# Optimization experiments

Measured on AMD Instinct MI355X. Metric: run time of the kernel, lower is better.

The kernel has to match this reference:

```python
import jax, jax.numpy as jnp
import numpy as np

B, D, H, C = 128, 512, 1024, 1000


def setup_inputs() -> dict:
    key = jax.random.key(0)
    k1, k2, k3 = jax.random.split(key, 3)
    x = jax.random.normal(k1, (B, D), dtype=jnp.float32)
    W1 = jax.random.normal(k2, (D, H), dtype=jnp.float32) * (1.0 / np.sqrt(D))
    b1 = jnp.zeros((H,), dtype=jnp.float32)
    W2 = jax.random.normal(k3, (H, C), dtype=jnp.float32) * (1.0 / np.sqrt(H))
    b2 = jnp.zeros((C,), dtype=jnp.float32)
    return {"x": x, "W1": W1, "b1": b1, "W2": W2, "b2": b2, "step": 0}


def _logits(W1, b1, W2, b2, xi):
    # 2-layer MLP forward for a single sample xi: [D] -> [C]
    h = jnp.maximum(xi @ W1 + b1, 0.0)
    return h @ W2 + b2


def _per_sample_loss(params, xi, key):
    W1, b1, W2, b2 = params
    logit = _logits(W1, b1, W2, b2, xi)  # [C]
    # model samples a label from its own softmax (multinomial); sampling is
    # non-differentiable, matching torch's multinomial -> stop_gradient
    y = jax.random.categorical(key, jax.lax.stop_gradient(logit))
    return -jax.nn.log_softmax(logit)[y]  # CrossEntropyLoss on 1 sample


def reference(x, W1, b1, W2, b2, step):
    params = (W1, b1, W2, b2)
    keys = jax.random.split(jax.random.key(42), x.shape[0])
    # vmap(grad(loss)) -> per-sample gradients for every parameter
    grads = jax.vmap(jax.grad(_per_sample_loss), in_axes=(None, 0, 0))(params, x, keys)
    n = jnp.asarray(x.shape[0], dtype=x.dtype)
    # trace_p = sum_b ||g_b||^2 / B for each parameter
    traces = [jnp.sum(g * g) / n for g in grads]
    overall = traces[0] + traces[1] + traces[2] + traces[3]
    return jnp.stack([overall] + traces)  # [5]: overall, W1, b1, W2, b2
```

## Files before the change

kernel.cpp:

```cpp
#include <hip/hip_runtime.h>
#include <hip/hip_bf16.h>
#include <stdint.h>
#include <math.h>

#define B_N 128
#define D_N 512
#define H_N 1024
#define C_N 1000
#define CP  1024

__device__ __forceinline__ uint32_t rotl32(uint32_t v, int r) {
  return (v << r) | (v >> (32 - r));
}

__device__ __forceinline__ void threefry2x32(uint32_t k0, uint32_t k1,
                                             uint32_t x0, uint32_t x1,
                                             uint32_t &o0, uint32_t &o1) {
  uint32_t ks2 = k0 ^ k1 ^ 0x1BD11BDAu;
#define TF_R(r) { x0 += x1; x1 = rotl32(x1, r); x1 ^= x0; }
  x0 += k0; x1 += k1;
  TF_R(13) TF_R(15) TF_R(26) TF_R(6)
  x0 += k1; x1 += ks2 + 1u;
  TF_R(17) TF_R(29) TF_R(16) TF_R(24)
  x0 += ks2; x1 += k0 + 2u;
  TF_R(13) TF_R(15) TF_R(26) TF_R(6)
  x0 += k0; x1 += k1 + 3u;
  TF_R(17) TF_R(29) TF_R(16) TF_R(24)
  x0 += k1; x1 += ks2 + 4u;
  TF_R(13) TF_R(15) TF_R(26) TF_R(6)
  x0 += ks2; x1 += k0 + 5u;
#undef TF_R
  o0 = x0; o1 = x1;
}

__device__ __forceinline__ float gumbel_from_key(uint32_t k0, uint32_t k1, uint32_t i) {
  uint32_t o0, o1;
  threefry2x32(k0, k1, 0u, i, o0, o1);
  uint32_t bits = o0 ^ o1;
  uint32_t fb = (bits >> 9) | 0x3f800000u;
  float f = __uint_as_float(fb) - 1.0f;
  const float tiny = 1.1754943508222875e-38f;
  float u = fmaxf(tiny, f * (1.0f - tiny) + tiny);
  return -logf(-logf(u));
}

__device__ __forceinline__ float block_sum512(float v, float* red) {
  #pragma unroll
  for (int o = 32; o; o >>= 1) v += __shfl_xor(v, o);
  __syncthreads();
  if ((threadIdx.x & 63) == 0) red[threadIdx.x >> 6] = v;
  __syncthreads();
  return red[0] + red[1] + red[2] + red[3] + red[4] + red[5] + red[6] + red[7];
}

__device__ __forceinline__ float block_max512(float v, float* red) {
  #pragma unroll
  for (int o = 32; o; o >>= 1) v = fmaxf(v, __shfl_xor(v, o));
  __syncthreads();
  if ((threadIdx.x & 63) == 0) red[threadIdx.x >> 6] = v;
  __syncthreads();
  float m = red[0];
  #pragma unroll
  for (int w = 1; w < 8; w++) m = fmaxf(m, red[w]);
  return m;
}

__global__ __launch_bounds__(256) void k_fc1(const float* __restrict__ X,
                                             const float* __restrict__ W1,
                                             const float* __restrict__ b1,
                                             float* __restrict__ hpre) {
  __shared__ float xs[4 * D_N];
  int cbase = blockIdx.x * 128;
  int sbase = blockIdx.y * 4;
  int t = threadIdx.x;
  #pragma unroll
  for (int k = 0; k < 8; k++) {
    int idx = t + k * 256;
    int s = idx >> 9, d = idx & 511;
    xs[idx] = X[(sbase + s) * D_N + d];
  }
  __syncthreads();
  int c = cbase + (t & 127);
  int sq = t >> 7;
  const float* xp0 = &xs[(sq * 2 + 0) * D_N];
  const float* xp1 = &xs[(sq * 2 + 1) * D_N];
  float acc0 = 0.f, acc1 = 0.f;
  const float* W1c = W1 + c;
  for (int d0 = 0; d0 < D_N; d0 += 16) {
    float w[16];
    #pragma unroll
    for (int i = 0; i < 16; i++) w[i] = W1c[(d0 + i) * H_N];
    #pragma unroll
    for (int q = 0; q < 4; q++) {
      float4 xa = *reinterpret_cast<const float4*>(&xp0[d0 + q * 4]);
      float4 xb = *reinterpret_cast<const float4*>(&xp1[d0 + q * 4]);
      acc0 += xa.x * w[q*4+0] + xa.y * w[q*4+1] + xa.z * w[q*4+2] + xa.w * w[q*4+3];
      acc1 += xb.x * w[q*4+0] + xb.y * w[q*4+1] + xb.z * w[q*4+2] + xb.w * w[q*4+3];
    }
  }
  float bb = b1[c];
  int s0 = sbase + sq * 2;
  hpre[(s0 + 0) * H_N + c] = acc0 + bb;
  hpre[(s0 + 1) * H_N + c] = acc1 + bb;
}

__global__ __launch_bounds__(256) void k_fc2(const float* __restrict__ hpre,
                                             const float* __restrict__ W2,
                                             float* __restrict__ logits_part) {
  __shared__ float hs[8 * 512];
  int cbase = blockIdx.x * 128;
  int sbase = blockIdx.y * 8;
  int kb = blockIdx.z;
  int t = threadIdx.x;
  #pragma unroll
  for (int k = 0; k < 16; k++) {
    int idx = t + k * 256;
    int s = idx >> 9, j = idx & 511;
    hs[idx] = fmaxf(hpre[(sbase + s) * H_N + kb * 512 + j], 0.0f);
  }
  __syncthreads();
  int c = cbase + (t & 127);
  int sq = t >> 7;
  if (c < C_N) {
    const float* hp0 = &hs[(sq * 4 + 0) * 512];
    const float* hp1 = &hs[(sq * 4 + 1) * 512];
    const float* hp2 = &hs[(sq * 4 + 2) * 512];
    const float* hp3 = &hs[(sq * 4 + 3) * 512];
    float a0 = 0.f, a1 = 0.f, a2 = 0.f, a3 = 0.f;
    const float* W2c = W2 + (size_t)(kb * 512) * C_N + c;
    for (int j0 = 0; j0 < 512; j0 += 8) {
      float w[8];
      #pragma unroll
      for (int i = 0; i < 8; i++) w[i] = W2c[(j0 + i) * C_N];
      #pragma unroll
      for (int q = 0; q < 2; q++) {
        float4 hA = *reinterpret_cast<const float4*>(&hp0[j0 + q * 4]);
        float4 hB = *reinterpret_cast<const float4*>(&hp1[j0 + q * 4]);
        float4 hC = *reinterpret_cast<const float4*>(&hp2[j0 + q * 4]);
        float4 hD = *reinterpret_cast<const float4*>(&hp3[j0 + q * 4]);
        a0 += hA.x * w[q*4+0] + hA.y * w[q*4+1] + hA.z * w[q*4+2] + hA.w * w[q*4+3];
        a1 += hB.x * w[q*4+0] + hB.y * w[q*4+1] + hB.z * w[q*4+2] + hB.w * w[q*4+3];
        a2 += hC.x * w[q*4+0] + hC.y * w[q*4+1] + hC.z * w[q*4+2] + hC.w * w[q*4+3];
        a3 += hD.x * w[q*4+0] + hD.y * w[q*4+1] + hD.z * w[q*4+2] + hD.w * w[q*4+3];
      }
    }
    float* lp = logits_part + (size_t)kb * (B_N * CP);
    int s0 = sbase + sq * 4;
    lp[(s0 + 0) * CP + c] = a0;
    lp[(s0 + 1) * CP + c] = a1;
    lp[(s0 + 2) * CP + c] = a2;
    lp[(s0 + 3) * CP + c] = a3;
  }
}

__global__ __launch_bounds__(512) void k_sample(const float* __restrict__ X,
                                                const float* __restrict__ hpre,
                                                const float* __restrict__ logits_part,
                                                const float* __restrict__ b2,
                                                float* __restrict__ g,
                                                float* __restrict__ xsq_out,
                                                float* __restrict__ samp_part) {
  __shared__ float lg[C_N];
  __shared__ float red[8];
  __shared__ float redv[8];
  __shared__ int   redi[8];
  __shared__ uint32_t keys[2];
  int b = blockIdx.x;
  int t = threadIdx.x;

  const float* p0 = logits_part;
  const float* p1 = logits_part + (B_N * CP);
  lg[t] = p0[b * CP + t] + p1[b * CP + t] + b2[t];
  if (t + 512 < C_N)
    lg[t + 512] = p0[b * CP + t + 512] + p1[b * CP + t + 512] + b2[t + 512];
  if (t == 0) {
    uint32_t o0, o1;
    threefry2x32(0u, 42u, 0u, (uint32_t)b, o0, o1);
    keys[0] = o0; keys[1] = o1;
  }
  __syncthreads();
  uint32_t k0 = keys[0], k1 = keys[1];

  float bz = -INFINITY; int bi = 0x7fffffff;
  {
    float z0 = lg[t] + gumbel_from_key(k0, k1, (uint32_t)t);
    bz = z0; bi = t;
    if (t + 512 < C_N) {
      float z1 = lg[t + 512] + gumbel_from_key(k0, k1, (uint32_t)(t + 512));
      if (z1 > bz || (z1 == bz && (t + 512) < bi)) { bz = z1; bi = t + 512; }
    }
  }
  #pragma unroll
  for (int o = 32; o; o >>= 1) {
    float ov = __shfl_xor(bz, o);
    int   oi = __shfl_xor(bi, o);
    if (ov > bz || (ov == bz && oi < bi)) { bz = ov; bi = oi; }
  }
  if ((t & 63) == 0) { redv[t >> 6] = bz; redi[t >> 6] = bi; }
  __syncthreads();
  if (t == 0) {
    #pragma unroll
    for (int w = 1; w < 8; w++) {
      if (redv[w] > redv[0] || (redv[w] == redv[0] && redi[w] < redi[0])) {
        redv[0] = redv[w]; redi[0] = redi[w];
      }
    }
  }
  __syncthreads();
  int y = redi[0];

  float lm = lg[t];
  if (t + 512 < C_N) lm = fmaxf(lm, lg[t + 512]);
  float m = block_max512(lm, red);
  float ea = expf(lg[t] - m);
  float eb = (t + 512 < C_N) ? expf(lg[t + 512] - m) : 0.0f;
  float sum1 = block_sum512(ea + eb, red);
  float inv = 1.0f / sum1;

  float ga  = ea * inv - ((t == y) ? 1.0f : 0.0f);
  float gb2 = eb * inv - (((t + 512) == y) ? 1.0f : 0.0f);
  g[b * CP + t] = ga;
  g[b * CP + t + 512] = (t + 512 < C_N) ? gb2 : 0.0f;
  float gn = ga * ga + ((t + 512 < C_N) ? gb2 * gb2 : 0.0f);
  float tnorm = block_sum512(gn, red);

  float h0 = fmaxf(hpre[b * H_N + t], 0.0f);
  float h1 = fmaxf(hpre[b * H_N + t + 512], 0.0f);
  float hsq = block_sum512(h0 * h0 + h1 * h1, red);

  float xv = (t < D_N) ? X[b * D_N + t] : 0.0f;
  float xsq = block_sum512(xv * xv, red);

  if (t == 0) {
    xsq_out[b] = xsq;
    samp_part[b * 2 + 0] = hsq * tnorm;
    samp_part[b * 2 + 1] = tnorm;
  }
}

__global__ __launch_bounds__(512) void k_bwd1(const float* __restrict__ g,
                                              const float* __restrict__ W2,
                                              const float* __restrict__ hpre,
                                              const float* __restrict__ xsq,
                                              float* __restrict__ bwd_part) {
  __shared__ float gs[8 * 1024];
  __shared__ float xq[8];
  __shared__ float wred[8][2];
  int jb = blockIdx.x * 16;
  int sbase = blockIdx.y * 8;
  int t = threadIdx.x;
  #pragma unroll
  for (int k = 0; k < 16; k++) {
    int idx = t + k * 512;
    gs[idx] = g[(sbase + (idx >> 10)) * CP + (idx & 1023)];
  }
  if (t < 8) xq[t] = xsq[sbase + t];
  __syncthreads();

  int w = t >> 6, lane = t & 63;
  int j0 = jb + w * 2, j1 = j0 + 1;
  float a0[8] = {0,0,0,0,0,0,0,0};
  float a1[8] = {0,0,0,0,0,0,0,0};
  const float* w2r0 = W2 + (size_t)j0 * C_N;
  const float* w2r1 = W2 + (size_t)j1 * C_N;
  #pragma unroll
  for (int it = 0; it < 4; it++) {
    int c0 = it * 256 + lane * 4;
    bool act = (c0 < C_N);
    float4 wv0 = act ? *reinterpret_cast<const float4*>(w2r0 + c0)
                     : make_float4(0.f, 0.f, 0.f, 0.f);
    float4 wv1 = act ? *reinterpret_cast<const float4*>(w2r1 + c0)
                     : make_float4(0.f, 0.f, 0.f, 0.f);
    #pragma unroll
    for (int s = 0; s < 8; s++) {
      float4 gv = *reinterpret_cast<const float4*>(&gs[s * 1024 + c0]);
      a0[s] += wv0.x * gv.x + wv0.y * gv.y + wv0.z * gv.z + wv0.w * gv.w;
      a1[s] += wv1.x * gv.x + wv1.y * gv.y + wv1.z * gv.z + wv1.w * gv.w;
    }
  }
  #pragma unroll
  for (int off = 32; off; off >>= 1) {
    #pragma unroll
    for (int s = 0; s < 8; s++) {
      a0[s] += __shfl_xor(a0[s], off);
      a1[s] += __shfl_xor(a1[s], off);
    }
  }
  float cb = 0.f, cw = 0.f;
  #pragma unroll
  for (int s = 0; s < 8; s++) {
    float h0 = hpre[(sbase + s) * H_N + j0];
    float h1 = hpre[(sbase + s) * H_N + j1];
    float v0 = (h0 > 0.f) ? a0[s] : 0.f;
    float v1 = (h1 > 0.f) ? a1[s] : 0.f;
    float q = v0 * v0 + v1 * v1;
    cb += q;
    cw += xq[s] * q;
  }
  if (lane == 0) { wred[w][0] = cw; wred[w][1] = cb; }
  __syncthreads();
  if (t == 0) {
    float sw = 0.f, sb = 0.f;
    #pragma unroll
    for (int i = 0; i < 8; i++) { sw += wred[i][0]; sb += wred[i][1]; }
    int bid = blockIdx.y * 64 + blockIdx.x;
    bwd_part[bid * 2 + 0] = sw;
    bwd_part[bid * 2 + 1] = sb;
  }
}

__global__ __launch_bounds__(512) void k_final(const float* __restrict__ samp_part,
                                               const float* __restrict__ bwd_part,
                                               float* __restrict__ out) {
  __shared__ float red[8];
  int t = threadIdx.x;
  float w1v = bwd_part[t * 2 + 0] + bwd_part[(t + 512) * 2 + 0];
  float b1v = bwd_part[t * 2 + 1] + bwd_part[(t + 512) * 2 + 1];
  float w2v = (t < B_N) ? samp_part[t * 2 + 0] : 0.f;
  float b2v = (t < B_N) ? samp_part[t * 2 + 1] : 0.f;
  w1v = block_sum512(w1v, red);
  b1v = block_sum512(b1v, red);
  w2v = block_sum512(w2v, red);
  b2v = block_sum512(b2v, red);
  if (t == 0) {
    w1v /= 128.0f; b1v /= 128.0f; w2v /= 128.0f; b2v /= 128.0f;
    out[0] = w1v + b1v + w2v + b2v;
    out[1] = w1v;
    out[2] = b1v;
    out[3] = w2v;
    out[4] = b2v;
  }
}

extern "C" void kernel_launch(void* const* d_in, const int* in_sizes, int n_in,
                              void* d_out, int out_size, void* d_ws, size_t ws_size,
                              hipStream_t stream) {
  const float* X  = (const float*)d_in[0];
  const float* W1 = (const float*)d_in[1];
  const float* b1 = (const float*)d_in[2];
  const float* W2 = (const float*)d_in[3];
  const float* b2 = (const float*)d_in[4];
  float* out = (float*)d_out;

  float* ws        = (float*)d_ws;
  float* hpre      = ws;
  float* lpart     = hpre + 131072;
  float* g         = lpart + 262144;
  float* xsq       = g + 131072;
  float* samp_part = xsq + 128;
  float* bwd_part  = samp_part + 256;

  k_fc1<<<dim3(8, 32), 256, 0, stream>>>(X, W1, b1, hpre);
  k_fc2<<<dim3(8, 16, 2), 256, 0, stream>>>(hpre, W2, lpart);
  k_sample<<<B_N, 512, 0, stream>>>(X, hpre, lpart, b2, g, xsq, samp_part);
  k_bwd1<<<dim3(64, 16), 512, 0, stream>>>(g, W2, hpre, xsq, bwd_part);
  k_final<<<1, 512, 0, stream>>>(samp_part, bwd_part, out);
}
```

Measured before the change: 66.35 us.

## Split fc2 reduction into 8 K-partitions and double-buffer weight loads in fc1/fc2

fc2 now splits the hidden dimension into 8 partitions of 128 instead of 2 of 512, giving four times as many blocks. The sampling kernel sums 8 partial logit buffers. fc1 uses 512 threads with one sample per thread instead of two. Both GEMMs double-buffer weight registers to overlap global loads with FMAs. The trade is more partial-sum traffic and a larger workspace, in exchange for better parallelism and latency hiding.

Result: faster. 57.43 us (-13.4%).

```diff
diff --git a/kernel.cpp b/kernel.cpp
--- a/kernel.cpp
+++ b/kernel.cpp
@@ -8,6 +8,7 @@
 #define H_N 1024
 #define C_N 1000
 #define CP  1024
+#define NPART 8
 
 __device__ __forceinline__ uint32_t rotl32(uint32_t v, int r) {
   return (v << r) | (v >> (32 - r));
@@ -65,7 +66,7 @@
   return m;
 }
 
-__global__ __launch_bounds__(256) void k_fc1(const float* __restrict__ X,
+__global__ __launch_bounds__(512) void k_fc1(const float* __restrict__ X,
                                              const float* __restrict__ W1,
                                              const float* __restrict__ b1,
                                              float* __restrict__ hpre) {
@@ -74,83 +75,97 @@
   int sbase = blockIdx.y * 4;
   int t = threadIdx.x;
   #pragma unroll
-  for (int k = 0; k < 8; k++) {
-    int idx = t + k * 256;
-    int s = idx >> 9, d = idx & 511;
-    xs[idx] = X[(sbase + s) * D_N + d];
+  for (int k = 0; k < 4; k++) {
+    int idx = t + k * 512;
+    xs[idx] = X[(sbase + (idx >> 9)) * D_N + (idx & 511)];
   }
   __syncthreads();
   int c = cbase + (t & 127);
-  int sq = t >> 7;
-  const float* xp0 = &xs[(sq * 2 + 0) * D_N];
-  const float* xp1 = &xs[(sq * 2 + 1) * D_N];
-  float acc0 = 0.f, acc1 = 0.f;
+  const float* xp = &xs[(t >> 7) * D_N];
   const float* W1c = W1 + c;
-  for (int d0 = 0; d0 < D_N; d0 += 16) {
-    float w[16];
-    #pragma unroll
-    for (int i = 0; i < 16; i++) w[i] = W1c[(d0 + i) * H_N];
+  float wA[16], wB[16];
+  #pragma unroll
+  for (int i = 0; i < 16; i++) wA[i] = W1c[i * H_N];
+  float acc = 0.f;
+  for (int d0 = 0; d0 < D_N; d0 += 32) {
+    #pragma unroll
+    for (int i = 0; i < 16; i++) wB[i] = W1c[((d0 + 16 + i) & (D_N - 1)) * H_N];
     #pragma unroll
     for (int q = 0; q < 4; q++) {
-      float4 xa = *reinterpret_cast<const float4*>(&xp0[d0 + q * 4]);
-      float4 xb = *reinterpret_cast<const float4*>(&xp1[d0 + q * 4]);
-      acc0 += xa.x * w[q*4+0] + xa.y * w[q*4+1] + xa.z * w[q*4+2] + xa.w * w[q*4+3];
-      acc1 += xb.x * w[q*4+0] + xb.y * w[q*4+1] + xb.z * w[q*4+2] + xb.w * w[q*4+3];
-    }
-  }
-  float bb = b1[c];
-  int s0 = sbase + sq * 2;
-  hpre[(s0 + 0) * H_N + c] = acc0 + bb;
-  hpre[(s0 + 1) * H_N + c] = acc1 + bb;
+      float4 xa = *reinterpret_cast<const float4*>(&xp[d0 + q * 4]);
+      acc += xa.x * wA[q*4+0] + xa.y * wA[q*4+1] + xa.z * wA[q*4+2] + xa.w * wA[q*4+3];
+    }
+    #pragma unroll
+    for (int i = 0; i < 16; i++) wA[i] = W1c[((d0 + 32 + i) & (D_N - 1)) * H_N];
+    #pragma unroll
+    for (int q = 0; q < 4; q++) {
+      float4 xa = *reinterpret_cast<const float4*>(&xp[d0 + 16 + q * 4]);
+      acc += xa.x * wB[q*4+0] + xa.y * wB[q*4+1] + xa.z * wB[q*4+2] + xa.w * wB[q*4+3];
+    }
+  }
+  hpre[(sbase + (t >> 7)) * H_N + c] = acc + b1[c];
 }
 
 __global__ __launch_bounds__(256) void k_fc2(const float* __restrict__ hpre,
                                              const float* __restrict__ W2,
                                              float* __restrict__ logits_part) {
-  __shared__ float hs[8 * 512];
+  __shared__ float hs[8 * 128];
   int cbase = blockIdx.x * 128;
   int sbase = blockIdx.y * 8;
   int kb = blockIdx.z;
   int t = threadIdx.x;
   #pragma unroll
-  for (int k = 0; k < 16; k++) {
+  for (int k = 0; k < 4; k++) {
     int idx = t + k * 256;
-    int s = idx >> 9, j = idx & 511;
-    hs[idx] = fmaxf(hpre[(sbase + s) * H_N + kb * 512 + j], 0.0f);
+    hs[idx] = fmaxf(hpre[(sbase + (idx >> 7)) * H_N + kb * 128 + (idx & 127)], 0.0f);
   }
   __syncthreads();
   int c = cbase + (t & 127);
+  if (c >= C_N) return;
   int sq = t >> 7;
-  if (c < C_N) {
-    const float* hp0 = &hs[(sq * 4 + 0) * 512];
-    const float* hp1 = &hs[(sq * 4 + 1) * 512];
-    const float* hp2 = &hs[(sq * 4 + 2) * 512];
-    const float* hp3 = &hs[(sq * 4 + 3) * 512];
-    float a0 = 0.f, a1 = 0.f, a2 = 0.f, a3 = 0.f;
-    const float* W2c = W2 + (size_t)(kb * 512) * C_N + c;
-    for (int j0 = 0; j0 < 512; j0 += 8) {
-      float w[8];
-      #pragma unroll
-      for (int i = 0; i < 8; i++) w[i] = W2c[(j0 + i) * C_N];
-      #pragma unroll
-      for (int q = 0; q < 2; q++) {
-        float4 hA = *reinterpret_cast<const float4*>(&hp0[j0 + q * 4]);
-        float4 hB = *reinterpret_cast<const float4*>(&hp1[j0 + q * 4]);
-        float4 hC = *reinterpret_cast<const float4*>(&hp2[j0 + q * 4]);
-        float4 hD = *reinterpret_cast<const float4*>(&hp3[j0 + q * 4]);
-        a0 += hA.x * w[q*4+0] + hA.y * w[q*4+1] + hA.z * w[q*4+2] + hA.w * w[q*4+3];
-        a1 += hB.x * w[q*4+0] + hB.y * w[q*4+1] + hB.z * w[q*4+2] + hB.w * w[q*4+3];
-        a2 += hC.x * w[q*4+0] + hC.y * w[q*4+1] + hC.z * w[q*4+2] + hC.w * w[q*4+3];
-        a3 += hD.x * w[q*4+0] + hD.y * w[q*4+1] + hD.z * w[q*4+2] + hD.w * w[q*4+3];
-      }
-    }
-    float* lp = logits_part + (size_t)kb * (B_N * CP);
-    int s0 = sbase + sq * 4;
-    lp[(s0 + 0) * CP + c] = a0;
-    lp[(s0 + 1) * CP + c] = a1;
-    lp[(s0 + 2) * CP + c] = a2;
-    lp[(s0 + 3) * CP + c] = a3;
-  }
+  const float* hp0 = &hs[(sq * 4 + 0) * 128];
+  const float* hp1 = &hs[(sq * 4 + 1) * 128];
+  const float* hp2 = &hs[(sq * 4 + 2) * 128];
+  const float* hp3 = &hs[(sq * 4 + 3) * 128];
+  const float* W2c = W2 + (size_t)(kb * 128) * C_N + c;
+  float wA[16], wB[16];
+  #pragma unroll
+  for (int i = 0; i < 16; i++) wA[i] = W2c[i * C_N];
+  float a0 = 0.f, a1 = 0.f, a2 = 0.f, a3 = 0.f;
+  for (int j0 = 0; j0 < 128; j0 += 32) {
+    #pragma unroll
+    for (int i = 0; i < 16; i++) wB[i] = W2c[((j0 + 16 + i) & 127) * C_N];
+    #pragma unroll
+    for (int q = 0; q < 4; q++) {
+      float4 hA = *reinterpret_cast<const float4*>(&hp0[j0 + q * 4]);
+      float4 hB = *reinterpret_cast<const float4*>(&hp1[j0 + q * 4]);
+      float4 hC = *reinterpret_cast<const float4*>(&hp2[j0 + q * 4]);
+      float4 hD = *reinterpret_cast<const float4*>(&hp3[j0 + q * 4]);
+      a0 += hA.x * wA[q*4+0] + hA.y * wA[q*4+1] + hA.z * wA[q*4+2] + hA.w * wA[q*4+3];
+      a1 += hB.x * wA[q*4+0] + hB.y * wA[q*4+1] + hB.z * wA[q*4+2] + hB.w * wA[q*4+3];
+      a2 += hC.x * wA[q*4+0] + hC.y * wA[q*4+1] + hC.z * wA[q*4+2] + hC.w * wA[q*4+3];
+      a3 += hD.x * wA[q*4+0] + hD.y * wA[q*4+1] + hD.z * wA[q*4+2] + hD.w * wA[q*4+3];
+    }
+    #pragma unroll
+    for (int i = 0; i < 16; i++) wA[i] = W2c[((j0 + 32 + i) & 127) * C_N];
+    #pragma unroll
+    for (int q = 0; q < 4; q++) {
+      float4 hA = *reinterpret_cast<const float4*>(&hp0[j0 + 16 + q * 4]);
+      float4 hB = *reinterpret_cast<const float4*>(&hp1[j0 + 16 + q * 4]);
+      float4 hC = *reinterpret_cast<const float4*>(&hp2[j0 + 16 + q * 4]);
+      float4 hD = *reinterpret_cast<const float4*>(&hp3[j0 + 16 + q * 4]);
+      a0 += hA.x * wB[q*4+0] + hA.y * wB[q*4+1] + hA.z * wB[q*4+2] + hA.w * wB[q*4+3];
+      a1 += hB.x * wB[q*4+0] + hB.y * wB[q*4+1] + hB.z * wB[q*4+2] + hB.w * wB[q*4+3];
+      a2 += hC.x * wB[q*4+0] + hC.y * wB[q*4+1] + hC.z * wB[q*4+2] + hC.w * wB[q*4+3];
+      a3 += hD.x * wB[q*4+0] + hD.y * wB[q*4+1] + hD.z * wB[q*4+2] + hD.w * wB[q*4+3];
+    }
+  }
+  float* lp = logits_part + (size_t)kb * (B_N * CP);
+  int s0 = sbase + sq * 4;
+  lp[(s0 + 0) * CP + c] = a0;
+  lp[(s0 + 1) * CP + c] = a1;
+  lp[(s0 + 2) * CP + c] = a2;
+  lp[(s0 + 3) * CP + c] = a3;
 }
 
 __global__ __launch_bounds__(512) void k_sample(const float* __restrict__ X,
@@ -168,11 +183,18 @@
   int b = blockIdx.x;
   int t = threadIdx.x;
 
-  const float* p0 = logits_part;
-  const float* p1 = logits_part + (B_N * CP);
-  lg[t] = p0[b * CP + t] + p1[b * CP + t] + b2[t];
-  if (t + 512 < C_N)
-    lg[t + 512] = p0[b * CP + t + 512] + p1[b * CP + t + 512] + b2[t + 512];
+  {
+    float sA = b2[t];
+    float sB = (t + 512 < C_N) ? b2[t + 512] : 0.f;
+    #pragma unroll
+    for (int p = 0; p < NPART; p++) {
+      const float* lp = logits_part + (size_t)p * (B_N * CP) + b * CP;
+      sA += lp[t];
+      if (t + 512 < C_N) sB += lp[t + 512];
+    }
+    lg[t] = sA;
+    if (t + 512 < C_N) lg[t + 512] = sB;
+  }
   if (t == 0) {
     uint32_t o0, o1;
     threefry2x32(0u, 42u, 0u, (uint32_t)b, o0, o1);
@@ -345,13 +367,13 @@
   float* ws        = (float*)d_ws;
   float* hpre      = ws;
   float* lpart     = hpre + 131072;
-  float* g         = lpart + 262144;
+  float* g         = lpart + NPART * 131072;
   float* xsq       = g + 131072;
   float* samp_part = xsq + 128;
   float* bwd_part  = samp_part + 256;
 
-  k_fc1<<<dim3(8, 32), 256, 0, stream>>>(X, W1, b1, hpre);
-  k_fc2<<<dim3(8, 16, 2), 256, 0, stream>>>(hpre, W2, lpart);
+  k_fc1<<<dim3(8, 32), 512, 0, stream>>>(X, W1, b1, hpre);
+  k_fc2<<<dim3(8, 16, NPART), 256, 0, stream>>>(hpre, W2, lpart);
   k_sample<<<B_N, 512, 0, stream>>>(X, hpre, lpart, b2, g, xsq, samp_part);
   k_bwd1<<<dim3(64, 16), 512, 0, stream>>>(g, W2, hpre, xsq, bwd_part);
   k_final<<<1, 512, 0, stream>>>(samp_part, bwd_part, out);
```

## Fuse sampling, backward and final reduction into one kernel with atomic last-block finish

Applied to the files above, without the earlier changes.

Merges the sampling, backward projection and final-reduction kernels into one kernel. Each block recomputes softmax and gumbel sampling for its 8 samples from the split-K logit partials, then does the W2 backward for 64 hidden units. A last-block atomic counter performs the final sum, and the x-norm computation moves into fc1. fc2 is retiled to 8-way split-K with transposed shared-memory h, float4 W2 loads and register double-buffering, and fc1 gains prefetching. This removes two launches and the g round-trip through global memory, at the cost of 16x redundant softmax and sampling work and more logit partial traffic.

After: 101.8 us. +53.4%, slower.

```diff
diff --git a/kernel.cpp b/kernel.cpp
--- a/kernel.cpp
+++ b/kernel.cpp
@@ -8,6 +8,8 @@
 #define H_N 1024
 #define C_N 1000
 #define CP  1024
+#define NJT 8
+#define LP_STRIDE (B_N * CP)
 
 __device__ __forceinline__ uint32_t rotl32(uint32_t v, int r) {
   return (v << r) | (v >> (32 - r));
@@ -44,6 +46,12 @@
   return -logf(-logf(u));
 }
 
+__device__ __forceinline__ float wave_sum(float v) {
+  #pragma unroll
+  for (int o = 32; o; o >>= 1) v += __shfl_xor(v, o);
+  return v;
+}
+
 __device__ __forceinline__ float block_sum512(float v, float* red) {
   #pragma unroll
   for (int o = 32; o; o >>= 1) v += __shfl_xor(v, o);
@@ -53,282 +61,271 @@
   return red[0] + red[1] + red[2] + red[3] + red[4] + red[5] + red[6] + red[7];
 }
 
-__device__ __forceinline__ float block_max512(float v, float* red) {
-  #pragma unroll
-  for (int o = 32; o; o >>= 1) v = fmaxf(v, __shfl_xor(v, o));
-  __syncthreads();
-  if ((threadIdx.x & 63) == 0) red[threadIdx.x >> 6] = v;
-  __syncthreads();
-  float m = red[0];
-  #pragma unroll
-  for (int w = 1; w < 8; w++) m = fmaxf(m, red[w]);
-  return m;
+__device__ __forceinline__ void fma4(float4 &a, const float4 &b, float s) {
+  a.x += b.x * s; a.y += b.y * s; a.z += b.z * s; a.w += b.w * s;
 }
 
 __global__ __launch_bounds__(256) void k_fc1(const float* __restrict__ X,
                                              const float* __restrict__ W1,
                                              const float* __restrict__ b1,
-                                             float* __restrict__ hpre) {
+                                             float* __restrict__ hfinal,
+                                             float* __restrict__ xsq,
+                                             unsigned int* __restrict__ counter) {
   __shared__ float xs[4 * D_N];
-  int cbase = blockIdx.x * 128;
-  int sbase = blockIdx.y * 4;
+  int bid = blockIdx.x;
+  int ct = bid & 7, sg = bid >> 3;
+  int cbase = ct * 128, sbase = sg * 4;
+  int t = threadIdx.x;
+  if (bid == 0 && t == 0) *counter = 0u;
+  #pragma unroll
+  for (int k = 0; k < 2; k++) {
+    int idx4 = t + k * 256;
+    int s = idx4 >> 7, dq = idx4 & 127;
+    *reinterpret_cast<float4*>(&xs[s * D_N + dq * 4]) =
+        *reinterpret_cast<const float4*>(&X[(sbase + s) * D_N + dq * 4]);
+  }
+  __syncthreads();
+
+  int c0 = cbase + (t & 127);
+  int spair = (t >> 7) * 2;
+  const float* W1c = W1 + c0;
+  const float* x0p = &xs[(spair + 0) * D_N];
+  const float* x1p = &xs[(spair + 1) * D_N];
+  float a0 = 0.f, a1 = 0.f;
+  float wA[8], wB[8];
+  #pragma unroll
+  for (int i = 0; i < 8; i++) wA[i] = W1c[(size_t)i * H_N];
+  for (int d0 = 0; d0 < D_N; d0 += 16) {
+    #pragma unroll
+    for (int i = 0; i < 8; i++) wB[i] = W1c[(size_t)((d0 + 8 + i) & (D_N - 1)) * H_N];
+    #pragma unroll
+    for (int i = 0; i < 8; i++) { a0 += wA[i] * x0p[d0 + i]; a1 += wA[i] * x1p[d0 + i]; }
+    #pragma unroll
+    for (int i = 0; i < 8; i++) wA[i] = W1c[(size_t)((d0 + 16 + i) & (D_N - 1)) * H_N];
+    #pragma unroll
+    for (int i = 0; i < 8; i++) { a0 += wB[i] * x0p[d0 + 8 + i]; a1 += wB[i] * x1p[d0 + 8 + i]; }
+  }
+  float bb = b1[c0];
+  hfinal[(size_t)(sbase + spair + 0) * H_N + c0] = a0 + bb;
+  hfinal[(size_t)(sbase + spair + 1) * H_N + c0] = a1 + bb;
+
+  if (ct == 0) {
+    int s = t >> 6, l = t & 63;
+    float v = 0.f;
+    #pragma unroll
+    for (int k = 0; k < 8; k++) { float xv = xs[s * D_N + l + k * 64]; v += xv * xv; }
+    v = wave_sum(v);
+    if (l == 0) xsq[sbase + s] = v;
+  }
+}
+
+__global__ __launch_bounds__(256) void k_fc2(const float* __restrict__ hfinal,
+                                             const float* __restrict__ W2,
+                                             float* __restrict__ lpart) {
+  __shared__ float hT[128 * 20];
+  int bid = blockIdx.x;
+  int ct = bid & 3, sg = (bid >> 2) & 7, jt = bid >> 5;
+  int cbase = ct * 256, sbase = sg * 16, jbase = jt * 128;
   int t = threadIdx.x;
   #pragma unroll
   for (int k = 0; k < 8; k++) {
     int idx = t + k * 256;
-    int s = idx >> 9, d = idx & 511;
-    xs[idx] = X[(sbase + s) * D_N + d];
-  }
-  __syncthreads();
-  int c = cbase + (t & 127);
-  int sq = t >> 7;
-  const float* xp0 = &xs[(sq * 2 + 0) * D_N];
-  const float* xp1 = &xs[(sq * 2 + 1) * D_N];
-  float acc0 = 0.f, acc1 = 0.f;
-  const float* W1c = W1 + c;
-  for (int d0 = 0; d0 < D_N; d0 += 16) {
-    float w[16];
-    #pragma unroll
-    for (int i = 0; i < 16; i++) w[i] = W1c[(d0 + i) * H_N];
-    #pragma unroll
-    for (int q = 0; q < 4; q++) {
-      float4 xa = *reinterpret_cast<const float4*>(&xp0[d0 + q * 4]);
-      float4 xb = *reinterpret_cast<const float4*>(&xp1[d0 + q * 4]);
-      acc0 += xa.x * w[q*4+0] + xa.y * w[q*4+1] + xa.z * w[q*4+2] + xa.w * w[q*4+3];
-      acc1 += xb.x * w[q*4+0] + xb.y * w[q*4+1] + xb.z * w[q*4+2] + xb.w * w[q*4+3];
-    }
-  }
-  float bb = b1[c];
-  int s0 = sbase + sq * 2;
-  hpre[(s0 + 0) * H_N + c] = acc0 + bb;
-  hpre[(s0 + 1) * H_N + c] = acc1 + bb;
-}
-
-__global__ __launch_bounds__(256) void k_fc2(const float* __restrict__ hpre,
-                                             const float* __restrict__ W2,
-                                             float* __restrict__ logits_part) {
-  __shared__ float hs[8 * 512];
-  int cbase = blockIdx.x * 128;
-  int sbase = blockIdx.y * 8;
-  int kb = blockIdx.z;
-  int t = threadIdx.x;
+    int s = idx >> 7, j = idx & 127;
+    hT[j * 20 + s] = fmaxf(hfinal[(size_t)(sbase + s) * H_N + jbase + j], 0.0f);
+  }
+  __syncthreads();
+  int c4 = cbase + (t & 63) * 4;
+  int s4 = (t >> 6) * 4;
+  int cr = (c4 <= C_N - 4) ? c4 : (C_N - 4);
+  float4 acc0 = {0,0,0,0}, acc1 = {0,0,0,0}, acc2 = {0,0,0,0}, acc3 = {0,0,0,0};
+  const float* W2c = W2 + (size_t)jbase * C_N + cr;
+  float4 wb[4], wn[4];
+  #pragma unroll
+  for (int i = 0; i < 4; i++)
+    wb[i] = *reinterpret_cast<const float4*>(W2c + (size_t)i * C_N);
+  for (int j0 = 0; j0 < 128; j0 += 4) {
+    #pragma unroll
+    for (int i = 0; i < 4; i++) {
+      int jn = j0 + 4 + i; jn = (jn < 128) ? jn : 127;
+      wn[i] = *reinterpret_cast<const float4*>(W2c + (size_t)jn * C_N);
+    }
+    #pragma unroll
+    for (int i = 0; i < 4; i++) {
+      float4 xv = *reinterpret_cast<const float4*>(&hT[(j0 + i) * 20 + s4]);
+      fma4(acc0, wb[i], xv.x);
+      fma4(acc1, wb[i], xv.y);
+      fma4(acc2, wb[i], xv.z);
+      fma4(acc3, wb[i], xv.w);
+    }
+    #pragma unroll
+    for (int i = 0; i < 4; i++) wb[i] = wn[i];
+  }
+  float* lp = lpart + (size_t)jt * LP_STRIDE;
+  *reinterpret_cast<float4*>(&lp[(size_t)(sbase + s4 + 0) * CP + c4]) = acc0;
+  *reinterpret_cast<float4*>(&lp[(size_t)(sbase + s4 + 1) * CP + c4]) = acc1;
+  *reinterpret_cast<float4*>(&lp[(size_t)(sbase + s4 + 2) * CP + c4]) = acc2;
+  *reinterpret_cast<float4*>(&lp[(size_t)(sbase + s4 + 3) * CP + c4]) = acc3;
+}
+
+__global__ __launch_bounds__(512) void k_mega(const float* __restrict__ lpart,
+                                              const float* __restrict__ b2,
+                                              const float* __restrict__ W2,
+                                              const float* __restrict__ hfinal,
+                                              const float* __restrict__ xsq_g,
+                                              float* __restrict__ samp_part,
+                                              float* __restrict__ bwd_part,
+                                              unsigned int* __restrict__ counter,
+                                              float* __restrict__ out) {
+  __shared__ float lg[8 * 1024];
+  __shared__ float tnormS[8], hsqS[8], xq[8];
+  __shared__ float wred[8][2];
+  __shared__ float red[8];
+  __shared__ int isLast;
+  int bid = blockIdx.x;
+  int sg = bid & 15, jt = bid >> 4;
+  int sbase = sg * 8, jbase = jt * 64;
+  int t = threadIdx.x, w = t >> 6, lane = t & 63;
+  int S = sbase + w;
+
+  uint32_t kk0, kk1;
+  threefry2x32(0u, 42u, 0u, (uint32_t)S, kk0, kk1);
+  float v[16];
+  float bz = -INFINITY; int bi = 0x7fffffff;
   #pragma unroll
   for (int k = 0; k < 16; k++) {
-    int idx = t + k * 256;
-    int s = idx >> 9, j = idx & 511;
-    hs[idx] = fmaxf(hpre[(sbase + s) * H_N + kb * 512 + j], 0.0f);
-  }
-  __syncthreads();
-  int c = cbase + (t & 127);
-  int sq = t >> 7;
-  if (c < C_N) {
-    const float* hp0 = &hs[(sq * 4 + 0) * 512];
-    const float* hp1 = &hs[(sq * 4 + 1) * 512];
-    const float* hp2 = &hs[(sq * 4 + 2) * 512];
-    const float* hp3 = &hs[(sq * 4 + 3) * 512];
-    float a0 = 0.f, a1 = 0.f, a2 = 0.f, a3 = 0.f;
-    const float* W2c = W2 + (size_t)(kb * 512) * C_N + c;
-    for (int j0 = 0; j0 < 512; j0 += 8) {
-      float w[8];
+    int c = lane + k * 64;
+    float val = -INFINITY;
+    if (c < C_N) {
+      val = b2[c];
       #pragma unroll
-      for (int i = 0; i < 8; i++) w[i] = W2c[(j0 + i) * C_N];
+      for (int p = 0; p < NJT; p++)
+        val += lpart[(size_t)p * LP_STRIDE + (size_t)S * CP + c];
+      float z = val + gumbel_from_key(kk0, kk1, (uint32_t)c);
+      if (z > bz || (z == bz && c < bi)) { bz = z; bi = c; }
+    }
+    v[k] = val;
+  }
+  #pragma unroll
+  for (int o = 32; o; o >>= 1) {
+    float ov = __shfl_xor(bz, o); int oi = __shfl_xor(bi, o);
+    if (ov > bz || (ov == bz && oi < bi)) { bz = ov; bi = oi; }
+  }
+  int y = bi;
+  float m = v[0];
+  #pragma unroll
+  for (int k = 1; k < 16; k++) m = fmaxf(m, v[k]);
+  #pragma unroll
+  for (int o = 32; o; o >>= 1) m = fmaxf(m, __shfl_xor(m, o));
+  float sum = 0.f;
+  #pragma unroll
+  for (int k = 0; k < 16; k++) { v[k] = expf(v[k] - m); sum += v[k]; }
+  sum = wave_sum(sum);
+  float inv = 1.0f / sum;
+  float tn = 0.f;
+  #pragma unroll
+  for (int k = 0; k < 16; k++) {
+    int c = lane + k * 64;
+    float gv = v[k] * inv - ((c == y) ? 1.0f : 0.0f);
+    if (c >= C_N) gv = 0.f;
+    lg[w * 1024 + c] = gv;
+    tn += gv * gv;
+  }
+  tn = wave_sum(tn);
+  if (lane == 0) tnormS[w] = tn;
+  if (t < 8) xq[t] = xsq_g[sbase + t];
+  if (jt == 0) {
+    float hv = 0.f;
+    #pragma unroll
+    for (int k = 0; k < 16; k++) {
+      float hh = hfinal[(size_t)S * H_N + lane + k * 64];
+      float r = fmaxf(hh, 0.f);
+      hv += r * r;
+    }
+    hv = wave_sum(hv);
+    if (lane == 0) hsqS[w] = hv;
+  }
+  __syncthreads();
+
+  float cb = 0.f, cw = 0.f;
+  for (int it2 = 0; it2 < 4; it2++) {
+    int jb = jbase + it2 * 16;
+    int j0 = jb + w * 2, j1 = j0 + 1;
+    float a0[8] = {0,0,0,0,0,0,0,0};
+    float a1[8] = {0,0,0,0,0,0,0,0};
+    const float* w2r0 = W2 + (size_t)j0 * C_N;
+    const float* w2r1 = W2 + (size_t)j1 * C_N;
+    #pragma unroll
+    for (int it = 0; it < 4; it++) {
+      int c0 = it * 256 + lane * 4;
+      bool act = (c0 < C_N);
+      float4 wv0 = act ? *reinterpret_cast<const float4*>(w2r0 + c0)
+                       : make_float4(0.f, 0.f, 0.f, 0.f);
+      float4 wv1 = act ? *reinterpret_cast<const float4*>(w2r1 + c0)
+                       : make_float4(0.f, 0.f, 0.f, 0.f);
       #pragma unroll
-      for (int q = 0; q < 2; q++) {
-        float4 hA = *reinterpret_cast<const float4*>(&hp0[j0 + q * 4]);
-        float4 hB = *reinterpret_cast<const float4*>(&hp1[j0 + q * 4]);
-        float4 hC = *reinterpret_cast<const float4*>(&hp2[j0 + q * 4]);
-        float4 hD = *reinterpret_cast<const float4*>(&hp3[j0 + q * 4]);
-        a0 += hA.x * w[q*4+0] + hA.y * w[q*4+1] + hA.z * w[q*4+2] + hA.w * w[q*4+3];
-        a1 += hB.x * w[q*4+0] + hB.y * w[q*4+1] + hB.z * w[q*4+2] + hB.w * w[q*4+3];
-        a2 += hC.x * w[q*4+0] + hC.y * w[q*4+1] + hC.z * w[q*4+2] + hC.w * w[q*4+3];
-        a3 += hD.x * w[q*4+0] + hD.y * w[q*4+1] + hD.z * w[q*4+2] + hD.w * w[q*4+3];
+      for (int s = 0; s < 8; s++) {
+        float4 gv = *reinterpret_cast<const float4*>(&lg[s * 1024 + c0]);
+        a0[s] += wv0.x * gv.x + wv0.y * gv.y + wv0.z * gv.z + wv0.w * gv.w;
+        a1[s] += wv1.x * gv.x + wv1.y * gv.y + wv1.z * gv.z + wv1.w * gv.w;
       }
     }
-    float* lp = logits_part + (size_t)kb * (B_N * CP);
-    int s0 = sbase + sq * 4;
-    lp[(s0 + 0) * CP + c] = a0;
-    lp[(s0 + 1) * CP + c] = a1;
-    lp[(s0 + 2) * CP + c] = a2;
-    lp[(s0 + 3) * CP + c] = a3;
-  }
-}
-
-__global__ __launch_bounds__(512) void k_sample(const float* __restrict__ X,
-                                                const float* __restrict__ hpre,
-                                                const float* __restrict__ logits_part,
-                                                const float* __restrict__ b2,
-                                                float* __restrict__ g,
-                                                float* __restrict__ xsq_out,
-                                                float* __restrict__ samp_part) {
-  __shared__ float lg[C_N];
-  __shared__ float red[8];
-  __shared__ float redv[8];
-  __shared__ int   redi[8];
-  __shared__ uint32_t keys[2];
-  int b = blockIdx.x;
-  int t = threadIdx.x;
-
-  const float* p0 = logits_part;
-  const float* p1 = logits_part + (B_N * CP);
-  lg[t] = p0[b * CP + t] + p1[b * CP + t] + b2[t];
-  if (t + 512 < C_N)
-    lg[t + 512] = p0[b * CP + t + 512] + p1[b * CP + t + 512] + b2[t + 512];
-  if (t == 0) {
-    uint32_t o0, o1;
-    threefry2x32(0u, 42u, 0u, (uint32_t)b, o0, o1);
-    keys[0] = o0; keys[1] = o1;
-  }
-  __syncthreads();
-  uint32_t k0 = keys[0], k1 = keys[1];
-
-  float bz = -INFINITY; int bi = 0x7fffffff;
-  {
-    float z0 = lg[t] + gumbel_from_key(k0, k1, (uint32_t)t);
-    bz = z0; bi = t;
-    if (t + 512 < C_N) {
-      float z1 = lg[t + 512] + gumbel_from_key(k0, k1, (uint32_t)(t + 512));
-      if (z1 > bz || (z1 == bz && (t + 512) < bi)) { bz = z1; bi = t + 512; }
-    }
-  }
-  #pragma unroll
-  for (int o = 32; o; o >>= 1) {
-    float ov = __shfl_xor(bz, o);
-    int   oi = __shfl_xor(bi, o);
-    if (ov > bz || (ov == bz && oi < bi)) { bz = ov; bi = oi; }
-  }
-  if ((t & 63) == 0) { redv[t >> 6] = bz; redi[t >> 6] = bi; }
-  __syncthreads();
-  if (t == 0) {
-    #pragma unroll
-    for (int w = 1; w < 8; w++) {
-      if (redv[w] > redv[0] || (redv[w] == redv[0] && redi[w] < redi[0])) {
-        redv[0] = redv[w]; redi[0] = redi[w];
+    #pragma unroll
+    for (int off = 32; off; off >>= 1) {
+      #pragma unroll
+      for (int s = 0; s < 8; s++) {
+        a0[s] += __shfl_xor(a0[s], off);
+        a1[s] += __shfl_xor(a1[s], off);
       }
     }
-  }
-  __syncthreads();
-  int y = redi[0];
-
-  float lm = lg[t];
-  if (t + 512 < C_N) lm = fmaxf(lm, lg[t + 512]);
-  float m = block_max512(lm, red);
-  float ea = expf(lg[t] - m);
-  float eb = (t + 512 < C_N) ? expf(lg[t + 512] - m) : 0.0f;
-  float sum1 = block_sum512(ea + eb, red);
-  float inv = 1.0f / sum1;
-
-  float ga  = ea * inv - ((t == y) ? 1.0f : 0.0f);
-  float gb2 = eb * inv - (((t + 512) == y) ? 1.0f : 0.0f);
-  g[b * CP + t] = ga;
-  g[b * CP + t + 512] = (t + 512 < C_N) ? gb2 : 0.0f;
-  float gn = ga * ga + ((t + 512 < C_N) ? gb2 * gb2 : 0.0f);
-  float tnorm = block_sum512(gn, red);
-
-  float h0 = fmaxf(hpre[b * H_N + t], 0.0f);
-  float h1 = fmaxf(hpre[b * H_N + t + 512], 0.0f);
-  float hsq = block_sum512(h0 * h0 + h1 * h1, red);
-
-  float xv = (t < D_N) ? X[b * D_N + t] : 0.0f;
-  float xsq = block_sum512(xv * xv, red);
-
-  if (t == 0) {
-    xsq_out[b] = xsq;
-    samp_part[b * 2 + 0] = hsq * tnorm;
-    samp_part[b * 2 + 1] = tnorm;
-  }
-}
-
-__global__ __launch_bounds__(512) void k_bwd1(const float* __restrict__ g,
-                                              const float* __restrict__ W2,
-                                              const float* __restrict__ hpre,
-                                              const float* __restrict__ xsq,
-                                              float* __restrict__ bwd_part) {
-  __shared__ float gs[8 * 1024];
-  __shared__ float xq[8];
-  __shared__ float wred[8][2];
-  int jb = blockIdx.x * 16;
-  int sbase = blockIdx.y * 8;
-  int t = threadIdx.x;
-  #pragma unroll
-  for (int k = 0; k < 16; k++) {
-    int idx = t + k * 512;
-    gs[idx] = g[(sbase + (idx >> 10)) * CP + (idx & 1023)];
-  }
-  if (t < 8) xq[t] = xsq[sbase + t];
-  __syncthreads();
-
-  int w = t >> 6, lane = t & 63;
-  int j0 = jb + w * 2, j1 = j0 + 1;
-  float a0[8] = {0,0,0,0,0,0,0,0};
-  float a1[8] = {0,0,0,0,0,0,0,0};
-  const float* w2r0 = W2 + (size_t)j0 * C_N;
-  const float* w2r1 = W2 + (size_t)j1 * C_N;
-  #pragma unroll
-  for (int it = 0; it < 4; it++) {
-    int c0 = it * 256 + lane * 4;
-    bool act = (c0 < C_N);
-    float4 wv0 = act ? *reinterpret_cast<const float4*>(w2r0 + c0)
-                     : make_float4(0.f, 0.f, 0.f, 0.f);
-    float4 wv1 = act ? *reinterpret_cast<const float4*>(w2r1 + c0)
-                     : make_float4(0.f, 0.f, 0.f, 0.f);
     #pragma unroll
     for (int s = 0; s < 8; s++) {
-      float4 gv = *reinterpret_cast<const float4*>(&gs[s * 1024 + c0]);
-      a0[s] += wv0.x * gv.x + wv0.y * gv.y + wv0.z * gv.z + wv0.w * gv.w;
-      a1[s] += wv1.x * gv.x + wv1.y * gv.y + wv1.z * gv.z + wv1.w * gv.w;
-    }
-  }
-  #pragma unroll
-  for (int off = 32; off; off >>= 1) {
-    #pragma unroll
-    for (int s = 0; s < 8; s++) {
-      a0[s] += __shfl_xor(a0[s], off);
-      a1[s] += __shfl_xor(a1[s], off);
-    }
-  }
-  float cb = 0.f, cw = 0.f;
-  #pragma unroll
-  for (int s = 0; s < 8; s++) {
-    float h0 = hpre[(sbase + s) * H_N + j0];
-    float h1 = hpre[(sbase + s) * H_N + j1];
-    float v0 = (h0 > 0.f) ? a0[s] : 0.f;
-    float v1 = (h1 > 0.f) ? a1[s] : 0.f;
-    float q = v0 * v0 + v1 * v1;
-    cb += q;
-    cw += xq[s] * q;
+      float h0 = hfinal[(size_t)(sbase + s) * H_N + j0];
+      float h1 = hfinal[(size_t)(sbase + s) * H_N + j1];
+      float v0 = (h0 > 0.f) ? a0[s] : 0.f;
+      float v1 = (h1 > 0.f) ? a1[s] : 0.f;
+      float q = v0 * v0 + v1 * v1;
+      cb += q;
+      cw += xq[s] * q;
+    }
   }
   if (lane == 0) { wred[w][0] = cw; wred[w][1] = cb; }
   __syncthreads();
+
   if (t == 0) {
     float sw = 0.f, sb = 0.f;
     #pragma unroll
     for (int i = 0; i < 8; i++) { sw += wred[i][0]; sb += wred[i][1]; }
-    int bid = blockIdx.y * 64 + blockIdx.x;
     bwd_part[bid * 2 + 0] = sw;
     bwd_part[bid * 2 + 1] = sb;
-  }
-}
-
-__global__ __launch_bounds__(512) void k_final(const float* __restrict__ samp_part,
-                                               const float* __restrict__ bwd_part,
-                                               float* __restrict__ out) {
-  __shared__ float red[8];
-  int t = threadIdx.x;
-  float w1v = bwd_part[t * 2 + 0] + bwd_part[(t + 512) * 2 + 0];
-  float b1v = bwd_part[t * 2 + 1] + bwd_part[(t + 512) * 2 + 1];
-  float w2v = (t < B_N) ? samp_part[t * 2 + 0] : 0.f;
-  float b2v = (t < B_N) ? samp_part[t * 2 + 1] : 0.f;
-  w1v = block_sum512(w1v, red);
-  b1v = block_sum512(b1v, red);
-  w2v = block_sum512(w2v, red);
-  b2v = block_sum512(b2v, red);
-  if (t == 0) {
-    w1v /= 128.0f; b1v /= 128.0f; w2v /= 128.0f; b2v /= 128.0f;
-    out[0] = w1v + b1v + w2v + b2v;
-    out[1] = w1v;
-    out[2] = b1v;
-    out[3] = w2v;
-    out[4] = b2v;
+    if (jt == 0) {
+      float s2 = 0.f, sb2 = 0.f;
+      #pragma unroll
+      for (int i = 0; i < 8; i++) { s2 += hsqS[i] * tnormS[i]; sb2 += tnormS[i]; }
+      samp_part[sg * 2 + 0] = s2;
+      samp_part[sg * 2 + 1] = sb2;
+    }
+    unsigned int old = __hip_atomic_fetch_add(counter, 1u, __ATOMIC_ACQ_REL,
+                                              __HIP_MEMORY_SCOPE_AGENT);
+    isLast = (old == 255u);
+  }
+  __syncthreads();
+  if (isLast) {
+    float w1v = (t < 256) ? bwd_part[t * 2 + 0] : 0.f;
+    float b1v = (t < 256) ? bwd_part[t * 2 + 1] : 0.f;
+    float w2v = (t < 16) ? samp_part[t * 2 + 0] : 0.f;
+    float b2v = (t < 16) ? samp_part[t * 2 + 1] : 0.f;
+    w1v = block_sum512(w1v, red);
+    b1v = block_sum512(b1v, red);
+    w2v = block_sum512(w2v, red);
+    b2v = block_sum512(b2v, red);
+    if (t == 0) {
+      w1v /= 128.0f; b1v /= 128.0f; w2v /= 128.0f; b2v /= 128.0f;
+      out[0] = w1v + b1v + w2v + b2v;
+      out[1] = w1v;
+      out[2] = b1v;
+      out[3] = w2v;
+      out[4] = b2v;
+    }
   }
 }
 
@@ -343,16 +340,15 @@
   float* out = (float*)d_out;
 
   float* ws        = (float*)d_ws;
-  float* hpre      = ws;
-  float* lpart     = hpre + 131072;
-  float* g         = lpart + 262144;
-  float* xsq       = g + 131072;
-  float* samp_part = xsq + 128;
-  float* bwd_part  = samp_part + 256;
-
-  k_fc1<<<dim3(8, 32), 256, 0, stream>>>(X, W1, b1, hpre);
-  k_fc2<<<dim3(8, 16, 2), 256, 0, stream>>>(hpre, W2, lpart);
-  k_sample<<<B_N, 512, 0, stream>>>(X, hpre, lpart, b2, g, xsq, samp_part);
-  k_bwd1<<<dim3(64, 16), 512, 0, stream>>>(g, W2, hpre, xsq, bwd_part);
-  k_final<<<1, 512, 0, stream>>>(samp_part, bwd_part, out);
-}
+  float* hfinal    = ws;
+  float* lpart     = hfinal + B_N * H_N;
+  float* xsq       = lpart + NJT * LP_STRIDE;
+  float* samp_part = xsq + B_N;
+  float* bwd_part  = samp_part + 32;
+  unsigned int* counter = (unsigned int*)(bwd_part + 512);
+
+  k_fc1<<<256, 256, 0, stream>>>(X, W1, b1, hfinal, xsq, counter);
+  k_fc2<<<256, 256, 0, stream>>>(hfinal, W2, lpart);
+  k_mega<<<256, 512, 0, stream>>>(lpart, b2, W2, hfinal, xsq,
+                                  samp_part, bwd_part, counter, out);
+}
```
